# Optimization experiments

Hardware: AMD Instinct MI355X
Metric: run time of the kernel (lower is better)

Reference implementation:

```python
import jax, jax.numpy as jnp
import numpy as np
from jax.scipy.special import gammaln, xlogy

B, S, C = 2, 2048, 1536
H, DK, DV = 8, 64, 192
F_REL = C // H  # 192 relative-position features


def positional_features_all(positions, feature_size, seq_length):
    # positions: [1, 2S-1] float32 (signed relative distances)
    n = feature_size // 6  # basis per class per sign
    ap = jnp.abs(positions)  # [1, 2S-1]
    Sf = float(seq_length)
    # exponential decay features
    max_range = float(np.log(Sf) / np.log(2.0))
    half_life = 2.0 ** jnp.linspace(3.0, max_range, n)  # min_half_life = 3.0
    feat_exp = jnp.exp(-jnp.log(2.0) / half_life * ap[..., None])
    # central mask features
    center_widths = 2.0 ** jnp.arange(1, n + 1, dtype=jnp.float32) - 1.0
    feat_cm = (center_widths > ap[..., None]).astype(jnp.float32)
    # gamma pdf features
    stddev = Sf / (2.0 * n)
    start_mean = Sf / n
    mean = jnp.linspace(start_mean, Sf, n)
    conc = (mean / stddev) ** 2
    rate = mean / (stddev ** 2)
    xg = ap[..., None]
    log_unnorm = xlogy(conc - 1.0, xg) - rate * xg
    log_norm = gammaln(conc) - conc * jnp.log(rate)
    prob = jnp.exp(log_unnorm - log_norm) + 1e-8
    feat_g = prob / jnp.max(prob, axis=1, keepdims=True)
    emb = jnp.concatenate([feat_exp, feat_cm, feat_g], axis=-1)  # [1, 2S-1, 3n]
    emb = jnp.concatenate([emb, jnp.sign(positions)[..., None] * emb], axis=-1)
    return emb  # [1, 2S-1, feature_size]


def relative_shift(x):
    # x: [B, H, T, 2T-1] -> [B, H, T, T] (Transformer-XL shift trick)
    b, h, t, _ = x.shape
    x = jnp.pad(x, ((0, 0), (0, 0), (0, 0), (1, 0)))  # [B,H,T,2T]
    x = x.reshape(b, h, 2 * t, t)[:, :, 1:, :]          # [B,H,2T-1,T]
    x = x.reshape(b, h, t, 2 * t - 1)[:, :, :, :t]      # [B,H,T,T]
    return x


def setup_inputs() -> dict:
    key = jax.random.key(0)
    ks = jax.random.split(key, 8)
    inp = {
        "x": jax.random.normal(ks[0], (B, S, C), dtype=jnp.float32),
        "mask": jax.random.randint(ks[1], (B, S), 0, 2, dtype=jnp.int32),
        "Wq": jax.random.normal(ks[2], (C, H * DK), dtype=jnp.float32) * 0.02,
        "Wk": jax.random.normal(ks[3], (C, H * DK), dtype=jnp.float32) * 0.02,
        "Wv": jax.random.normal(ks[4], (C, H * DV), dtype=jnp.float32) * 0.02,
        "Wr": jax.random.normal(ks[5], (F_REL, H * DK), dtype=jnp.float32) * 0.02,
        "r_w_bias": jax.random.normal(ks[6], (1, H, 1, DK), dtype=jnp.float32) * 0.02,
        "Wo": jax.random.normal(ks[7], (H * DV, H * DV), dtype=jnp.float32) * 0.02,
        "bo": jnp.zeros((H * DV,), dtype=jnp.float32),
    }
    return inp


def reference(x, mask, Wq, Wk, Wv, Wr, r_w_bias, Wo, bo):
    b, s, c = x.shape
    # projections -> [B, H, S, d]
    q = (x @ Wq).reshape(b, s, H, DK).transpose(0, 2, 1, 3) * (DK ** -0.5)
    k = (x @ Wk).reshape(b, s, H, DK).transpose(0, 2, 1, 3)
    v = (x @ Wv).reshape(b, s, H, DV).transpose(0, 2, 1, 3)
    # relative positional encodings for distances -S+1 .. S-1
    dist = jnp.arange(-s + 1, s, dtype=jnp.float32)[None, :]  # [1, 2S-1]
    pe = positional_features_all(dist, F_REL, s)               # [1, 2S-1, F_REL]
    r_k = (pe[0] @ Wr).reshape(2 * s - 1, H, DK).transpose(1, 0, 2)  # [H, 2S-1, DK]
    # content + position logits
    content_logits = jnp.einsum('bhqd,bhkd->bhqk', q, k)                   # [B,H,S,S]
    rel_logits = jnp.einsum('bhqd,hkd->bhqk', q + r_w_bias, r_k)           # [B,H,S,2S-1]
    logits = content_logits + relative_shift(rel_logits)
    logits = jnp.where(mask[:, None, None, :] == 0, -1e9, logits)
    weights = jax.nn.softmax(logits, axis=-1)
    out = jnp.einsum('bhqk,bhkd->bhqd', weights, v)  # [B,H,S,DV]
    out = out.transpose(0, 2, 1, 3).reshape(b, s, H * DV)
    return out @ Wo + bo
```

## Files before the change

### kernel.cpp

```cpp
#include <hip/hip_runtime.h>
#include <math.h>

#define SEQ 2048
#define CDIM 1536
#define HN 8
#define DVC 192
#define BN 2
#define NPOS 4095
#define HDK 512
#define HDV 1536
#define PSTR 72

typedef __attribute__((ext_vector_type(8))) _Float16 hf8v;
typedef __attribute__((ext_vector_type(4))) _Float16 hf4v;
typedef __attribute__((ext_vector_type(4))) float f4v;

static __device__ __forceinline__ f4v mfma16(hf8v a, hf8v b, f4v c) {
  return __builtin_amdgcn_mfma_f32_16x16x32_f16(a, b, c, 0, 0, 0);
}
static __device__ __forceinline__ void gl2lds16(const void* g, void* l) {
  __builtin_amdgcn_global_load_lds((const __attribute__((address_space(1))) unsigned int*)g,
                                   (__attribute__((address_space(3))) unsigned int*)l,
                                   16, 0, 0);
}
static __device__ __forceinline__ float rowmax16(float x) {
  x = fmaxf(x, __int_as_float(__builtin_amdgcn_update_dpp(0, __float_as_int(x), 0x128, 0xf, 0xf, true)));
  x = fmaxf(x, __int_as_float(__builtin_amdgcn_update_dpp(0, __float_as_int(x), 0x124, 0xf, 0xf, true)));
  x = fmaxf(x, __int_as_float(__builtin_amdgcn_update_dpp(0, __float_as_int(x), 0x122, 0xf, 0xf, true)));
  x = fmaxf(x, __int_as_float(__builtin_amdgcn_update_dpp(0, __float_as_int(x), 0x121, 0xf, 0xf, true)));
  return x;
}

#define PF_B   512
#define CAST_B 6144
#define TWQ_B  768
#define TWK_B  768
#define TWV_B  2304
#define TWO_B  2304
#define TWR_B  96
#define PREP_BLOCKS (PF_B + CAST_B + TWQ_B + TWK_B + TWV_B + TWO_B + TWR_B)

__device__ __forceinline__ void twc_tile(const float* __restrict__ W, _Float16* __restrict__ WT,
                                         int K, int N, int tile, float (*tls)[33], int tid) {
  int ntn = N >> 5;
  int nt = tile % ntn, kt = tile / ntn;
  int k0 = kt * 32, n0 = nt * 32;
  int tx = tid & 31, ty = tid >> 5;
#pragma unroll
  for (int p = 0; p < 4; p++) tls[ty + p * 8][tx] = W[(size_t)(k0 + ty + p * 8) * N + n0 + tx];
  __syncthreads();
#pragma unroll
  for (int p = 0; p < 4; p++) {
    int n = ty + p * 8;
    WT[(size_t)(n0 + n) * K + k0 + tx] = (_Float16)tls[tx][n];
  }
}

__global__ __launch_bounds__(256) void prep_kernel(
    const float* __restrict__ x, const float* __restrict__ Wq, const float* __restrict__ Wk,
    const float* __restrict__ Wv, const float* __restrict__ Wo, const float* __restrict__ Wr,
    float* __restrict__ pe_raw, unsigned* __restrict__ gmax, _Float16* __restrict__ xb,
    _Float16* __restrict__ WTqkv, _Float16* __restrict__ WoT, _Float16* __restrict__ WrT) {
  __shared__ float tls[32][33];
  int blk = blockIdx.x, tid = threadIdx.x;
  if (blk < PF_B) {
    int j = blk >> 4;
    int pos = (blk & 15) * 256 + tid;
    float prob = 0.0f;
    if (pos < NPOS) {
      float ap = fabsf((float)(pos - (SEQ - 1)));
      float hl = exp2f(3.0f + 8.0f * (float)j / 31.0f);
      float fe = exp2f(-ap / hl);
      float cw = exp2f((float)(j + 1)) - 1.0f;
      float fc = (cw > ap) ? 1.0f : 0.0f;
      float conc = 4.0f * (float)((j + 1) * (j + 1));
      float rate = (float)(j + 1) / 16.0f;
      float log_norm = lgammaf(conc) - conc * logf(rate);
      float log_un = (conc - 1.0f) * logf(ap) - rate * ap;
      prob = expf(log_un - log_norm) + 1e-8f;
      pe_raw[pos * 96 + j] = fe;
      pe_raw[pos * 96 + 32 + j] = fc;
      pe_raw[pos * 96 + 64 + j] = prob;
    }
    float m = prob;
#pragma unroll
    for (int off = 32; off > 0; off >>= 1) m = fmaxf(m, __shfl_down(m, off));
    __shared__ float red[4];
    if ((tid & 63) == 0) red[tid >> 6] = m;
    __syncthreads();
    if (tid == 0) {
      m = fmaxf(fmaxf(red[0], red[1]), fmaxf(red[2], red[3]));
      atomicMax(&gmax[j], __float_as_uint(m));
    }
  } else if (blk < PF_B + CAST_B) {
    int i = ((blk - PF_B) * 256 + tid) * 4;
    float4 v = *(const float4*)(x + i);
    _Float16 o[4] = {(_Float16)v.x, (_Float16)v.y, (_Float16)v.z, (_Float16)v.w};
    *(unsigned long long*)(xb + i) = *(const unsigned long long*)o;
  } else if (blk < PF_B + CAST_B + TWQ_B) {
    twc_tile(Wq, WTqkv + 0 * (size_t)CDIM, CDIM, HDK, blk - (PF_B + CAST_B), tls, tid);
  } else if (blk < PF_B + CAST_B + TWQ_B + TWK_B) {
    twc_tile(Wk, WTqkv + 512 * (size_t)CDIM, CDIM, HDK, blk - (PF_B + CAST_B + TWQ_B), tls, tid);
  } else if (blk < PF_B + CAST_B + TWQ_B + TWK_B + TWV_B) {
    twc_tile(Wv, WTqkv + 1024 * (size_t)CDIM, CDIM, HDV, blk - (PF_B + CAST_B + TWQ_B + TWK_B), tls, tid);
  } else if (blk < PF_B + CAST_B + TWQ_B + TWK_B + TWV_B + TWO_B) {
    twc_tile(Wo, WoT, CDIM, HDV, blk - (PF_B + CAST_B + TWQ_B + TWK_B + TWV_B), tls, tid);
  } else {
    twc_tile(Wr, WrT, 192, HDK, blk - (PF_B + CAST_B + TWQ_B + TWK_B + TWV_B + TWO_B), tls, tid);
  }
}

__global__ __launch_bounds__(256) void pe_norm_kernel(const float* __restrict__ pe_raw,
                                                      const unsigned* __restrict__ gmax,
                                                      _Float16* __restrict__ pe_h) {
  int idx = blockIdx.x * 256 + threadIdx.x;
  int pos = idx / 96, f = idx - pos * 96;
  float val = 0.0f, sval = 0.0f;
  if (pos < NPOS) {
    val = pe_raw[pos * 96 + f];
    if (f >= 64) val *= 1.0f / __uint_as_float(gmax[f - 64]);
    float sgn = (pos > SEQ - 1) ? 1.0f : ((pos < SEQ - 1) ? -1.0f : 0.0f);
    sval = sgn * val;
  }
  pe_h[pos * 192 + f] = (_Float16)val;
  pe_h[pos * 192 + 96 + f] = (_Float16)sval;
}

template <int MODE>
__global__ __launch_bounds__(256, 2) void mfma_gemm(
    const _Float16* __restrict__ A, const _Float16* __restrict__ B,
    const float* __restrict__ bias, void* __restrict__ out0, void* __restrict__ out1,
    void* __restrict__ out2, int K, int ntx) {
  __shared__ __align__(16) _Float16 As[128 * 64];
  __shared__ __align__(16) _Float16 Bs[128 * 64];
  const int tid = threadIdx.x;
  const int lane = tid & 63, l15 = lane & 15, quad = lane >> 4;
  const int wv = tid >> 6;
  const int wm = (wv & 1) * 64, wn = (wv >> 1) * 64;
  const int lin = blockIdx.x;
  const int cpx = gridDim.x >> 3;
  const int sw = (lin & 7) * cpx + (lin >> 3);
  const int row0 = (sw / ntx) * 128, col0 = (sw % ntx) * 128;
  f4v acc[4][4];
#pragma unroll
  for (int i = 0; i < 4; i++)
#pragma unroll
    for (int j = 0; j < 4; j++) acc[i][j] = (f4v)0.0f;

  for (int k0 = 0; k0 < K; k0 += 64) {
    __syncthreads();
#pragma unroll
    for (int p = 0; p < 4; p++) {
      int idx = tid + p * 256;
      int rr = idx >> 3, sc = idx & 7;
      int gc = (sc ^ (rr & 7)) << 3;
      gl2lds16(A + (size_t)(row0 + rr) * K + k0 + gc, As + idx * 8);
      gl2lds16(B + (size_t)(col0 + rr) * K + k0 + gc, Bs + idx * 8);
    }
    __syncthreads();
    hf8v af[4][2], bfr[4][2];
#pragma unroll
    for (int t = 0; t < 4; t++) {
      int lrA = wm + t * 16 + l15;
      int lrB = wn + t * 16 + l15;
#pragma unroll
      for (int kc = 0; kc < 2; kc++) {
        af[t][kc]  = *(const hf8v*)(As + lrA * 64 + ((((kc << 2) | quad) ^ (lrA & 7)) << 3));
        bfr[t][kc] = *(const hf8v*)(Bs + lrB * 64 + ((((kc << 2) | quad) ^ (lrB & 7)) << 3));
      }
    }
#pragma unroll
    for (int kc = 0; kc < 2; kc++)
#pragma unroll
      for (int mt = 0; mt < 4; mt++)
#pragma unroll
        for (int nt = 0; nt < 4; nt++)
          acc[mt][nt] = mfma16(af[mt][kc], bfr[nt][kc], acc[mt][nt]);
  }
#pragma unroll
  for (int mt = 0; mt < 4; mt++)
#pragma unroll
    for (int reg = 0; reg < 4; reg++) {
      int r = row0 + wm + mt * 16 + quad * 4 + reg;
      int bb = r >> 11, ss = r & (SEQ - 1);
#pragma unroll
      for (int nt = 0; nt < 4; nt++) {
        int c = col0 + wn + nt * 16 + l15;
        float vv = acc[mt][nt][reg];
        if (MODE == 0) {
          if (c < 512) {
            ((_Float16*)out0)[(size_t)r * HDK + c] = (_Float16)(vv * 0.125f);
          } else if (c < 1024) {
            int cc = c - 512, h = cc >> 6, d = cc & 63;
            ((_Float16*)out1)[(((size_t)bb * HN + h) * SEQ + ss) * 64 + d] = (_Float16)vv;
          } else {
            int cc = c - 1024, h = cc / DVC, e = cc - h * DVC;
            int jp = (ss & ~63) | ((ss & 15) << 2) | ((ss >> 4) & 3);
            ((_Float16*)out2)[(((size_t)bb * HN + h) * DVC + e) * SEQ + jp] = (_Float16)vv;
          }
        } else if (MODE == 1) {
          int h = c >> 6, d = c & 63;
          ((_Float16*)out0)[((size_t)h * 4096 + r) * 64 + d] = (_Float16)vv;
        } else {
          ((float*)out0)[(size_t)r * HDV + c] = vv + bias[c];
        }
      }
    }
}

template <bool SPLITKV>
__global__ __launch_bounds__(256, 2) void attn_mfma(
    const _Float16* __restrict__ qb, const _Float16* __restrict__ kb,
    const _Float16* __restrict__ vtb, const _Float16* __restrict__ rkb,
    const float* __restrict__ rwb, const int* __restrict__ mask,
    _Float16* __restrict__ attn_out, float* __restrict__ Opart, float* __restrict__ ml) {
  __shared__ __align__(16) _Float16 Vts[192 * 64];
  __shared__ __align__(16) _Float16 RKs[192 * 64];
  __shared__ __align__(16) _Float16 Kts[64 * 64];
  __shared__ __align__(16) _Float16 Pbs[128 * PSTR];

  const int lin = blockIdx.x;
  const int chunk = SPLITKV ? 64 : 32;
  const int swz = (lin & 7) * chunk + (lin >> 3);
  const int bx = swz & 15;
  const int by = swz >> 4;
  const int i0 = bx * 128;
  const int bh = SPLITKV ? (by & 15) : by;
  const int half = SPLITKV ? (by >> 4) : 0;
  const int b = bh >> 3, h = bh & 7;
  const int tid = threadIdx.x;
  const int wv = tid >> 6, lane = tid & 63;
  const int l15 = lane & 15, quad = lane >> 4;

  hf8v qf[2][2], qbf[2][2];
#pragma unroll
  for (int s = 0; s < 2; s++) {
    int qrow = i0 + wv * 32 + s * 16 + l15;
    const _Float16* qp = qb + (size_t)(b * SEQ + qrow) * HDK + h * 64;
#pragma unroll
    for (int kc = 0; kc < 2; kc++) {
      hf8v qv = *(const hf8v*)(qp + kc * 32 + quad * 8);
      qf[s][kc] = qv;
      hf8v t;
#pragma unroll
      for (int j = 0; j < 8; j++)
        t[j] = (_Float16)((float)qv[j] + rwb[h * 64 + kc * 32 + quad * 8 + j]);
      qbf[s][kc] = t;
    }
  }

  f4v Of[2][12];
#pragma unroll
  for (int s = 0; s < 2; s++)
#pragma unroll
    for (int se = 0; se < 12; se++) Of[s][se] = (f4v)0.0f;
  float m_i[2][4] = {{-INFINITY, -INFINITY, -INFINITY, -INFINITY},
                     {-INFINITY, -INFINITY, -INFINITY, -INFINITY}};
  float l_i[2][4] = {{0.f, 0.f, 0.f, 0.f}, {0.f, 0.f, 0.f, 0.f}};

  const int j0beg = SPLITKV ? half * (SEQ / 2) : 0;
  const int j0end = SPLITKV ? j0beg + SEQ / 2 : SEQ;

  for (int j0 = j0beg; j0 < j0end; j0 += 64) {
    __syncthreads();
    int mraw[4];
#pragma unroll
    for (int st = 0; st < 4; st++) mraw[st] = mask[b * SEQ + j0 + st * 16 + l15];
    {
      const int U0 = j0 - i0 + 1920;
#pragma unroll
      for (int r = 0; r < 2; r++) {
        int idx = tid + r * 256, row = idx >> 3, sc = idx & 7;
        gl2lds16(kb + ((size_t)bh * SEQ + j0 + row) * 64 + ((sc ^ (row & 7)) << 3), Kts + idx * 8);
      }
#pragma unroll
      for (int r = 0; r < 6; r++) {
        int idx = tid + r * 256, row = idx >> 3, sc = idx & 7;
        gl2lds16(rkb + ((size_t)h * 4096 + U0 + row) * 64 + ((sc ^ (row & 7)) << 3), RKs + idx * 8);
      }
#pragma unroll
      for (int r = 0; r < 6; r++) {
        int idx = tid + r * 256, row = idx >> 3, sc = idx & 7;
        gl2lds16(vtb + ((size_t)bh * DVC + row) * SEQ + j0 + ((sc ^ (row & 7)) << 3), Vts + idx * 8);
      }
    }
    asm volatile("s_waitcnt vmcnt(6)" ::: "memory");
    __builtin_amdgcn_s_barrier();
    __builtin_amdgcn_sched_barrier(0);
    float mv[4];
#pragma unroll
    for (int st = 0; st < 4; st++) mv[st] = mraw[st] ? 0.f : -1e9f;

#pragma unroll
    for (int s = 0; s < 2; s++) {
      __builtin_amdgcn_s_setprio(1);
      f4v Sf[4];
#pragma unroll
      for (int st = 0; st < 4; st++) {
        Sf[st] = (f4v)0.0f;
#pragma unroll
        for (int kc = 0; kc < 2; kc++) {
          int row = st * 16 + l15;
          hf8v kf = *(const hf8v*)(Kts + row * 64 + ((((kc << 2) | quad) ^ (row & 7)) << 3));
          Sf[st] = mfma16(qf[s][kc], kf, Sf[st]);
        }
      }
      f4v Rf[5];
      const int tb = 112 - 32 * wv - 16 * s;
#pragma unroll
      for (int u = 0; u < 5; u++) {
        Rf[u] = (f4v)0.0f;
#pragma unroll
        for (int kc = 0; kc < 2; kc++) {
          int row = tb + u * 16 + l15;
          hf8v rf = *(const hf8v*)(RKs + row * 64 + ((((kc << 2) | quad) ^ (row & 7)) << 3));
          Rf[u] = mfma16(qbf[s][kc], rf, Rf[u]);
        }
      }
      __builtin_amdgcn_s_setprio(0);
#pragma unroll
      for (int reg = 0; reg < 4; reg++) {
        int delta = l15 - (quad << 2) - reg + 15;
        int srcl = (quad << 4) | (delta & 15);
        float sh0 = __shfl(Rf[0][reg], srcl, 64);
        float sh1 = __shfl(Rf[1][reg], srcl, 64);
        float sh2 = __shfl(Rf[2][reg], srcl, 64);
        float sh3 = __shfl(Rf[3][reg], srcl, 64);
        float sh4 = __shfl(Rf[4][reg], srcl, 64);
        bool hib = delta >= 16;
        Sf[0][reg] += (hib ? sh1 : sh0) + mv[0];
        Sf[1][reg] += (hib ? sh2 : sh1) + mv[1];
        Sf[2][reg] += (hib ? sh3 : sh2) + mv[2];
        Sf[3][reg] += (hib ? sh4 : sh3) + mv[3];
      }
#pragma unroll
      for (int reg = 0; reg < 4; reg++) {
        float t = fmaxf(fmaxf(Sf[0][reg], Sf[1][reg]), fmaxf(Sf[2][reg], Sf[3][reg]));
        t = rowmax16(t);
        if (__any(t - m_i[s][reg] > 8.0f)) {
          float mn = fmaxf(m_i[s][reg], t);
          float alpha = __expf(m_i[s][reg] - mn);
          m_i[s][reg] = mn;
          l_i[s][reg] *= alpha;
#pragma unroll
          for (int se = 0; se < 12; se++) Of[s][se][reg] *= alpha;
        }
        float mcur = m_i[s][reg];
        hf4v pv;
        float rs = 0.f;
#pragma unroll
        for (int st = 0; st < 4; st++) {
          float p = __expf(Sf[st][reg] - mcur);
          rs += p;
          pv[st] = (_Float16)p;
        }
        l_i[s][reg] += rs;
        *(hf4v*)(Pbs + (size_t)(wv * 32 + s * 16 + quad * 4 + reg) * PSTR + l15 * 4) = pv;
      }
    }

    hf8v pa[2][2];
#pragma unroll
    for (int s = 0; s < 2; s++)
#pragma unroll
      for (int kc = 0; kc < 2; kc++)
        pa[s][kc] = *(const hf8v*)(Pbs + (size_t)(wv * 32 + s * 16 + l15) * PSTR +
                                   kc * 32 + quad * 8);
    asm volatile("s_waitcnt vmcnt(0)" ::: "memory");
    __builtin_amdgcn_s_barrier();
    __builtin_amdgcn_sched_barrier(0);
    __builtin_amdgcn_s_setprio(1);
#pragma unroll
    for (int se = 0; se < 12; se++) {
#pragma unroll
      for (int kc = 0; kc < 2; kc++) {
        int row = se * 16 + l15;
        hf8v vf = *(const hf8v*)(Vts + row * 64 + ((((kc << 2) | quad) ^ (row & 7)) << 3));
        Of[0][se] = mfma16(pa[0][kc], vf, Of[0][se]);
        Of[1][se] = mfma16(pa[1][kc], vf, Of[1][se]);
      }
    }
    __builtin_amdgcn_s_setprio(0);
  }

#pragma unroll
  for (int s = 0; s < 2; s++)
#pragma unroll
    for (int reg = 0; reg < 4; reg++) {
      float ls = l_i[s][reg];
      ls += __shfl_xor(ls, 1);
      ls += __shfl_xor(ls, 2);
      ls += __shfl_xor(ls, 4);
      ls += __shfl_xor(ls, 8);
      int row = i0 + wv * 32 + s * 16 + quad * 4 + reg;
      int rg = b * SEQ + row;
      if constexpr (SPLITKV) {
        float* Op = Opart + ((size_t)(half * 4096 + rg)) * HDV + h * DVC;
#pragma unroll
        for (int se = 0; se < 12; se++) Op[se * 16 + l15] = Of[s][se][reg];
        if (l15 == 0) {
          size_t mlb = (((size_t)half * 4096 + rg) * HN + h) * 2;
          ml[mlb] = m_i[s][reg];
          ml[mlb + 1] = ls;
        }
      } else {
        float inv = 1.0f / ls;
        size_t base2 = (size_t)rg * HDV + h * DVC;
#pragma unroll
        for (int se = 0; se < 12; se++)
          attn_out[base2 + se * 16 + l15] = (_Float16)(Of[s][se][reg] * inv);
      }
    }
}

__global__ __launch_bounds__(256) void combine_kernel(const float* __restrict__ Opart,
                                                      const float* __restrict__ ml,
                                                      _Float16* __restrict__ attn_out) {
  int i4 = blockIdx.x * 256 + threadIdx.x;
  int rg = i4 / 384, c4 = (i4 - rg * 384) * 4;
  int h = c4 / DVC;
  size_t mlb0 = ((size_t)rg * HN + h) * 2;
  size_t mlb1 = (((size_t)4096 + rg) * HN + h) * 2;
  float m0 = ml[mlb0], l0 = ml[mlb0 + 1];
  float m1 = ml[mlb1], l1 = ml[mlb1 + 1];
  float M = fmaxf(m0, m1);
  float w0 = __expf(m0 - M), w1 = __expf(m1 - M);
  float inv = 1.0f / (l0 * w0 + l1 * w1);
  float4 O0 = *(const float4*)(Opart + (size_t)rg * HDV + c4);
  float4 O1 = *(const float4*)(Opart + ((size_t)4096 + rg) * HDV + c4);
  _Float16 o[4] = {(_Float16)((O0.x * w0 + O1.x * w1) * inv),
                   (_Float16)((O0.y * w0 + O1.y * w1) * inv),
                   (_Float16)((O0.z * w0 + O1.z * w1) * inv),
                   (_Float16)((O0.w * w0 + O1.w * w1) * inv)};
  *(unsigned long long*)(attn_out + (size_t)rg * HDV + c4) = *(const unsigned long long*)o;
}

extern "C" void kernel_launch(void* const* d_in, const int* in_sizes, int n_in,
                              void* d_out, int out_size, void* d_ws, size_t ws_size,
                              hipStream_t stream) {
  const float* x    = (const float*)d_in[0];
  const int*   mask = (const int*)d_in[1];
  const float* Wq   = (const float*)d_in[2];
  const float* Wk   = (const float*)d_in[3];
  const float* Wv   = (const float*)d_in[4];
  const float* Wr   = (const float*)d_in[5];
  const float* rwb  = (const float*)d_in[6];
  const float* Wo   = (const float*)d_in[7];
  const float* bo   = (const float*)d_in[8];
  float* out = (float*)d_out;

  char* wsb = (char*)d_ws;
  size_t o = 0;
  auto al = [](size_t v) { return (v + 255) & ~(size_t)255; };
#define CARVE(ptr_t, name, bytes) ptr_t name = (ptr_t)(wsb + o); o = al(o + (bytes));
  CARVE(float*, pe_raw, (size_t)4096 * 96 * 4)
  CARVE(unsigned*, gmax, 128)
  CARVE(_Float16*, pe_h, (size_t)4096 * 192 * 2)
  CARVE(_Float16*, WrT, (size_t)HDK * 192 * 2)
  CARVE(_Float16*, xb, (size_t)BN * SEQ * CDIM * 2)
  CARVE(_Float16*, WTqkv, (size_t)2560 * CDIM * 2)
  CARVE(_Float16*, WoT, (size_t)HDV * CDIM * 2)
  CARVE(_Float16*, qb, (size_t)BN * SEQ * HDK * 2)
  CARVE(_Float16*, kb, (size_t)BN * SEQ * HDK * 2)
  CARVE(_Float16*, vtb, (size_t)BN * SEQ * HDV * 2)
  CARVE(_Float16*, rkb, (size_t)HN * 4096 * 64 * 2)
  _Float16* attnh = xb;
  CARVE(float*, Opart, (size_t)2 * 4096 * HDV * 4)
  CARVE(float*, ml, (size_t)2 * 4096 * HN * 2 * 4)
  bool dosplit = (o <= ws_size);

  hipMemsetAsync(gmax, 0, 32 * sizeof(unsigned), stream);
  prep_kernel<<<PREP_BLOCKS, 256, 0, stream>>>(x, Wq, Wk, Wv, Wo, Wr, pe_raw, gmax, xb,
                                               WTqkv, WoT, WrT);
  pe_norm_kernel<<<4096 * 96 / 256, 256, 0, stream>>>(pe_raw, gmax, pe_h);
  mfma_gemm<0><<<640, 256, 0, stream>>>(xb, WTqkv, nullptr, qb, kb, vtb, CDIM, 20);
  mfma_gemm<1><<<128, 256, 0, stream>>>(pe_h, WrT, nullptr, rkb, nullptr, nullptr, 192, 4);
  if (dosplit) {
    attn_mfma<true><<<512, 256, 0, stream>>>(qb, kb, vtb, rkb, rwb, mask,
                                             attnh, Opart, ml);
    combine_kernel<<<4096 * 384 / 256, 256, 0, stream>>>(Opart, ml, attnh);
  } else {
    attn_mfma<false><<<256, 256, 0, stream>>>(qb, kb, vtb, rkb, rwb, mask,
                                              attnh, nullptr, nullptr);
  }
  mfma_gemm<2><<<384, 256, 0, stream>>>(attnh, WoT, bo, out, nullptr, nullptr, CDIM, 12);
}
```

Before: 301.8 us.

## Compute positional features analytically, store split partials in fp16, tune GEMM occupancy

Drops the pe_raw buffer, the atomic max reduction and the memset by computing the gamma-pdf normaliser analytically from the distribution mode, so positional features are made in a single kernel. The split-KV attention partials are normalised and stored as fp16 instead of fp32, which halves the partial-output traffic, and the combine kernel is simplified to match. The GEMM raises its launch-bounds occupancy hint to 3 blocks and loads LDS fragments per k-chunk to cut register pressure. Risks: fp16 partials lose some precision, and the analytic max only matches the true max over integer distances if the mode clamping is exact.

```diff
diff --git a/kernel.cpp b/kernel.cpp
--- a/kernel.cpp
+++ b/kernel.cpp
@@ -31,14 +31,13 @@
   return x;
 }
 
-#define PF_B   512
 #define CAST_B 6144
 #define TWQ_B  768
 #define TWK_B  768
 #define TWV_B  2304
 #define TWO_B  2304
 #define TWR_B  96
-#define PREP_BLOCKS (PF_B + CAST_B + TWQ_B + TWK_B + TWV_B + TWO_B + TWR_B)
+#define PREP_BLOCKS (CAST_B + TWQ_B + TWK_B + TWV_B + TWO_B + TWR_B)
 
 __device__ __forceinline__ void twc_tile(const float* __restrict__ W, _Float16* __restrict__ WT,
                                          int K, int N, int tile, float (*tls)[33], int tid) {
@@ -59,66 +58,53 @@
 __global__ __launch_bounds__(256) void prep_kernel(
     const float* __restrict__ x, const float* __restrict__ Wq, const float* __restrict__ Wk,
     const float* __restrict__ Wv, const float* __restrict__ Wo, const float* __restrict__ Wr,
-    float* __restrict__ pe_raw, unsigned* __restrict__ gmax, _Float16* __restrict__ xb,
-    _Float16* __restrict__ WTqkv, _Float16* __restrict__ WoT, _Float16* __restrict__ WrT) {
+    _Float16* __restrict__ xb, _Float16* __restrict__ WTqkv, _Float16* __restrict__ WoT,
+    _Float16* __restrict__ WrT) {
   __shared__ float tls[32][33];
   int blk = blockIdx.x, tid = threadIdx.x;
-  if (blk < PF_B) {
-    int j = blk >> 4;
-    int pos = (blk & 15) * 256 + tid;
-    float prob = 0.0f;
-    if (pos < NPOS) {
-      float ap = fabsf((float)(pos - (SEQ - 1)));
-      float hl = exp2f(3.0f + 8.0f * (float)j / 31.0f);
-      float fe = exp2f(-ap / hl);
-      float cw = exp2f((float)(j + 1)) - 1.0f;
-      float fc = (cw > ap) ? 1.0f : 0.0f;
-      float conc = 4.0f * (float)((j + 1) * (j + 1));
-      float rate = (float)(j + 1) / 16.0f;
-      float log_norm = lgammaf(conc) - conc * logf(rate);
-      float log_un = (conc - 1.0f) * logf(ap) - rate * ap;
-      prob = expf(log_un - log_norm) + 1e-8f;
-      pe_raw[pos * 96 + j] = fe;
-      pe_raw[pos * 96 + 32 + j] = fc;
-      pe_raw[pos * 96 + 64 + j] = prob;
-    }
-    float m = prob;
-#pragma unroll
-    for (int off = 32; off > 0; off >>= 1) m = fmaxf(m, __shfl_down(m, off));
-    __shared__ float red[4];
-    if ((tid & 63) == 0) red[tid >> 6] = m;
-    __syncthreads();
-    if (tid == 0) {
-      m = fmaxf(fmaxf(red[0], red[1]), fmaxf(red[2], red[3]));
-      atomicMax(&gmax[j], __float_as_uint(m));
-    }
-  } else if (blk < PF_B + CAST_B) {
-    int i = ((blk - PF_B) * 256 + tid) * 4;
+  if (blk < CAST_B) {
+    int i = (blk * 256 + tid) * 4;
     float4 v = *(const float4*)(x + i);
     _Float16 o[4] = {(_Float16)v.x, (_Float16)v.y, (_Float16)v.z, (_Float16)v.w};
     *(unsigned long long*)(xb + i) = *(const unsigned long long*)o;
-  } else if (blk < PF_B + CAST_B + TWQ_B) {
-    twc_tile(Wq, WTqkv + 0 * (size_t)CDIM, CDIM, HDK, blk - (PF_B + CAST_B), tls, tid);
-  } else if (blk < PF_B + CAST_B + TWQ_B + TWK_B) {
-    twc_tile(Wk, WTqkv + 512 * (size_t)CDIM, CDIM, HDK, blk - (PF_B + CAST_B + TWQ_B), tls, tid);
-  } else if (blk < PF_B + CAST_B + TWQ_B + TWK_B + TWV_B) {
-    twc_tile(Wv, WTqkv + 1024 * (size_t)CDIM, CDIM, HDV, blk - (PF_B + CAST_B + TWQ_B + TWK_B), tls, tid);
-  } else if (blk < PF_B + CAST_B + TWQ_B + TWK_B + TWV_B + TWO_B) {
-    twc_tile(Wo, WoT, CDIM, HDV, blk - (PF_B + CAST_B + TWQ_B + TWK_B + TWV_B), tls, tid);
+  } else if (blk < CAST_B + TWQ_B) {
+    twc_tile(Wq, WTqkv + 0 * (size_t)CDIM, CDIM, HDK, blk - CAST_B, tls, tid);
+  } else if (blk < CAST_B + TWQ_B + TWK_B) {
+    twc_tile(Wk, WTqkv + 512 * (size_t)CDIM, CDIM, HDK, blk - (CAST_B + TWQ_B), tls, tid);
+  } else if (blk < CAST_B + TWQ_B + TWK_B + TWV_B) {
+    twc_tile(Wv, WTqkv + 1024 * (size_t)CDIM, CDIM, HDV, blk - (CAST_B + TWQ_B + TWK_B), tls, tid);
+  } else if (blk < CAST_B + TWQ_B + TWK_B + TWV_B + TWO_B) {
+    twc_tile(Wo, WoT, CDIM, HDV, blk - (CAST_B + TWQ_B + TWK_B + TWV_B), tls, tid);
   } else {
-    twc_tile(Wr, WrT, 192, HDK, blk - (PF_B + CAST_B + TWQ_B + TWK_B + TWV_B + TWO_B), tls, tid);
-  }
-}
-
-__global__ __launch_bounds__(256) void pe_norm_kernel(const float* __restrict__ pe_raw,
-                                                      const unsigned* __restrict__ gmax,
-                                                      _Float16* __restrict__ pe_h) {
+    twc_tile(Wr, WrT, 192, HDK, blk - (CAST_B + TWQ_B + TWK_B + TWV_B + TWO_B), tls, tid);
+  }
+}
+
+__global__ __launch_bounds__(256) void pe_kernel(_Float16* __restrict__ pe_h) {
   int idx = blockIdx.x * 256 + threadIdx.x;
   int pos = idx / 96, f = idx - pos * 96;
   float val = 0.0f, sval = 0.0f;
   if (pos < NPOS) {
-    val = pe_raw[pos * 96 + f];
-    if (f >= 64) val *= 1.0f / __uint_as_float(gmax[f - 64]);
+    float ap = fabsf((float)(pos - (SEQ - 1)));
+    int j = f & 31, cls = f >> 5;
+    if (cls == 0) {
+      float hl = exp2f(3.0f + 8.0f * (float)j / 31.0f);
+      val = exp2f(-ap / hl);
+    } else if (cls == 1) {
+      float cw = exp2f((float)(j + 1)) - 1.0f;
+      val = (cw > ap) ? 1.0f : 0.0f;
+    } else {
+      float conc = 4.0f * (float)((j + 1) * (j + 1));
+      float rate = (float)(j + 1) / 16.0f;
+      float log_norm = lgammaf(conc) - conc * logf(rate);
+      float pv = expf((conc - 1.0f) * logf(ap) - rate * ap - log_norm) + 1e-8f;
+      float mode = (conc - 1.0f) / rate;
+      float a0 = fminf(floorf(mode), 2047.0f);
+      float a1 = fminf(a0 + 1.0f, 2047.0f);
+      float p0 = expf((conc - 1.0f) * logf(a0) - rate * a0 - log_norm) + 1e-8f;
+      float p1 = expf((conc - 1.0f) * logf(a1) - rate * a1 - log_norm) + 1e-8f;
+      val = pv / fmaxf(p0, p1);
+    }
     float sgn = (pos > SEQ - 1) ? 1.0f : ((pos < SEQ - 1) ? -1.0f : 0.0f);
     sval = sgn * val;
   }
@@ -127,7 +113,7 @@
 }
 
 template <int MODE>
-__global__ __launch_bounds__(256, 2) void mfma_gemm(
+__global__ __launch_bounds__(256, 3) void mfma_gemm(
     const _Float16* __restrict__ A, const _Float16* __restrict__ B,
     const float* __restrict__ bias, void* __restrict__ out0, void* __restrict__ out1,
     void* __restrict__ out2, int K, int ntx) {
@@ -158,24 +144,22 @@
       gl2lds16(B + (size_t)(col0 + rr) * K + k0 + gc, Bs + idx * 8);
     }
     __syncthreads();
-    hf8v af[4][2], bfr[4][2];
-#pragma unroll
-    for (int t = 0; t < 4; t++) {
-      int lrA = wm + t * 16 + l15;
-      int lrB = wn + t * 16 + l15;
-#pragma unroll
-      for (int kc = 0; kc < 2; kc++) {
-        af[t][kc]  = *(const hf8v*)(As + lrA * 64 + ((((kc << 2) | quad) ^ (lrA & 7)) << 3));
-        bfr[t][kc] = *(const hf8v*)(Bs + lrB * 64 + ((((kc << 2) | quad) ^ (lrB & 7)) << 3));
-      }
-    }
-#pragma unroll
-    for (int kc = 0; kc < 2; kc++)
+#pragma unroll
+    for (int kc = 0; kc < 2; kc++) {
+      hf8v af[4], bfr[4];
+#pragma unroll
+      for (int t = 0; t < 4; t++) {
+        int lrA = wm + t * 16 + l15;
+        int lrB = wn + t * 16 + l15;
+        af[t]  = *(const hf8v*)(As + lrA * 64 + ((((kc << 2) | quad) ^ (lrA & 7)) << 3));
+        bfr[t] = *(const hf8v*)(Bs + lrB * 64 + ((((kc << 2) | quad) ^ (lrB & 7)) << 3));
+      }
 #pragma unroll
       for (int mt = 0; mt < 4; mt++)
 #pragma unroll
         for (int nt = 0; nt < 4; nt++)
-          acc[mt][nt] = mfma16(af[mt][kc], bfr[nt][kc], acc[mt][nt]);
+          acc[mt][nt] = mfma16(af[mt], bfr[nt], acc[mt][nt]);
+    }
   }
 #pragma unroll
   for (int mt = 0; mt < 4; mt++)
@@ -213,7 +197,7 @@
     const _Float16* __restrict__ qb, const _Float16* __restrict__ kb,
     const _Float16* __restrict__ vtb, const _Float16* __restrict__ rkb,
     const float* __restrict__ rwb, const int* __restrict__ mask,
-    _Float16* __restrict__ attn_out, float* __restrict__ Opart, float* __restrict__ ml) {
+    _Float16* __restrict__ attn_out, _Float16* __restrict__ Opart, float* __restrict__ ml) {
   __shared__ __align__(16) _Float16 Vts[192 * 64];
   __shared__ __align__(16) _Float16 RKs[192 * 64];
   __shared__ __align__(16) _Float16 Kts[64 * 64];
@@ -394,17 +378,17 @@
       ls += __shfl_xor(ls, 8);
       int row = i0 + wv * 32 + s * 16 + quad * 4 + reg;
       int rg = b * SEQ + row;
+      float inv = 1.0f / ls;
       if constexpr (SPLITKV) {
-        float* Op = Opart + ((size_t)(half * 4096 + rg)) * HDV + h * DVC;
-#pragma unroll
-        for (int se = 0; se < 12; se++) Op[se * 16 + l15] = Of[s][se][reg];
+        _Float16* Op = Opart + ((size_t)(half * 4096 + rg)) * HDV + h * DVC;
+#pragma unroll
+        for (int se = 0; se < 12; se++) Op[se * 16 + l15] = (_Float16)(Of[s][se][reg] * inv);
         if (l15 == 0) {
           size_t mlb = (((size_t)half * 4096 + rg) * HN + h) * 2;
           ml[mlb] = m_i[s][reg];
           ml[mlb + 1] = ls;
         }
       } else {
-        float inv = 1.0f / ls;
         size_t base2 = (size_t)rg * HDV + h * DVC;
 #pragma unroll
         for (int se = 0; se < 12; se++)
@@ -413,7 +397,7 @@
     }
 }
 
-__global__ __launch_bounds__(256) void combine_kernel(const float* __restrict__ Opart,
+__global__ __launch_bounds__(256) void combine_kernel(const _Float16* __restrict__ Opart,
                                                       const float* __restrict__ ml,
                                                       _Float16* __restrict__ attn_out) {
   int i4 = blockIdx.x * 256 + threadIdx.x;
@@ -424,15 +408,16 @@
   float m0 = ml[mlb0], l0 = ml[mlb0 + 1];
   float m1 = ml[mlb1], l1 = ml[mlb1 + 1];
   float M = fmaxf(m0, m1);
-  float w0 = __expf(m0 - M), w1 = __expf(m1 - M);
-  float inv = 1.0f / (l0 * w0 + l1 * w1);
-  float4 O0 = *(const float4*)(Opart + (size_t)rg * HDV + c4);
-  float4 O1 = *(const float4*)(Opart + ((size_t)4096 + rg) * HDV + c4);
-  _Float16 o[4] = {(_Float16)((O0.x * w0 + O1.x * w1) * inv),
-                   (_Float16)((O0.y * w0 + O1.y * w1) * inv),
-                   (_Float16)((O0.z * w0 + O1.z * w1) * inv),
-                   (_Float16)((O0.w * w0 + O1.w * w1) * inv)};
-  *(unsigned long long*)(attn_out + (size_t)rg * HDV + c4) = *(const unsigned long long*)o;
+  float w0 = l0 * __expf(m0 - M), w1 = l1 * __expf(m1 - M);
+  float inv = 1.0f / (w0 + w1);
+  w0 *= inv;
+  w1 *= inv;
+  hf4v O0 = *(const hf4v*)(Opart + (size_t)rg * HDV + c4);
+  hf4v O1 = *(const hf4v*)(Opart + ((size_t)4096 + rg) * HDV + c4);
+  hf4v o;
+#pragma unroll
+  for (int q = 0; q < 4; q++) o[q] = (_Float16)((float)O0[q] * w0 + (float)O1[q] * w1);
+  *(hf4v*)(attn_out + (size_t)rg * HDV + c4) = o;
 }
 
 extern "C" void kernel_launch(void* const* d_in, const int* in_sizes, int n_in,
@@ -453,8 +438,6 @@
   size_t o = 0;
   auto al = [](size_t v) { return (v + 255) & ~(size_t)255; };
 #define CARVE(ptr_t, name, bytes) ptr_t name = (ptr_t)(wsb + o); o = al(o + (bytes));
-  CARVE(float*, pe_raw, (size_t)4096 * 96 * 4)
-  CARVE(unsigned*, gmax, 128)
   CARVE(_Float16*, pe_h, (size_t)4096 * 192 * 2)
   CARVE(_Float16*, WrT, (size_t)HDK * 192 * 2)
   CARVE(_Float16*, xb, (size_t)BN * SEQ * CDIM * 2)
@@ -465,14 +448,12 @@
   CARVE(_Float16*, vtb, (size_t)BN * SEQ * HDV * 2)
   CARVE(_Float16*, rkb, (size_t)HN * 4096 * 64 * 2)
   _Float16* attnh = xb;
-  CARVE(float*, Opart, (size_t)2 * 4096 * HDV * 4)
+  CARVE(_Float16*, Opart, (size_t)2 * 4096 * HDV * 2)
   CARVE(float*, ml, (size_t)2 * 4096 * HN * 2 * 4)
   bool dosplit = (o <= ws_size);
 
-  hipMemsetAsync(gmax, 0, 32 * sizeof(unsigned), stream);
-  prep_kernel<<<PREP_BLOCKS, 256, 0, stream>>>(x, Wq, Wk, Wv, Wo, Wr, pe_raw, gmax, xb,
-                                               WTqkv, WoT, WrT);
-  pe_norm_kernel<<<4096 * 96 / 256, 256, 0, stream>>>(pe_raw, gmax, pe_h);
+  prep_kernel<<<PREP_BLOCKS, 256, 0, stream>>>(x, Wq, Wk, Wv, Wo, Wr, xb, WTqkv, WoT, WrT);
+  pe_kernel<<<4096 * 96 / 256, 256, 0, stream>>>(pe_h);
   mfma_gemm<0><<<640, 256, 0, stream>>>(xb, WTqkv, nullptr, qb, kb, vtb, CDIM, 20);
   mfma_gemm<1><<<128, 256, 0, stream>>>(pe_h, WrT, nullptr, rkb, nullptr, nullptr, 192, 4);
   if (dosplit) {
```

After: 306.7 us. About the same (+1.6%).
